# Kernel tuning notes

Hardware: AMD Instinct MI355X
Metric: run time of the kernel (lower is better)

The kernel has to match this reference:

```python
import jax, jax.numpy as jnp
import numpy as np

B, S, C = 8, 1024, 768
H = 12            # num_heads
HD = C // H       # head_dim = 64
QH = QW = 32      # input_size; QH*QW == S


def setup_inputs() -> dict:
    key = jax.random.key(0)
    ks = jax.random.split(key, 6)
    return {
        "x": jax.random.normal(ks[0], (B, S, C), dtype=jnp.float32),
        "w_qkv": jax.random.normal(ks[1], (3 * C, C), dtype=jnp.float32) * 0.02,
        "w_out": jax.random.normal(ks[2], (C, C), dtype=jnp.float32) * 0.02,
        "b_out": jax.random.normal(ks[3], (C,), dtype=jnp.float32) * 0.02,
        "rel_pos_h": jax.random.normal(ks[4], (2 * QH - 1, HD), dtype=jnp.float32) * 0.02,
        "rel_pos_w": jax.random.normal(ks[5], (2 * QW - 1, HD), dtype=jnp.float32) * 0.02,
    }


def reference(x, w_qkv, w_out, b_out, rel_pos_h, rel_pos_w):
    scale = HD ** -0.5
    # qkv projection (no bias), rearrange 'b s (qkv h d) -> qkv b h s d'
    qkv = (x @ w_qkv.T).reshape(B, S, 3, H, HD).transpose(2, 0, 3, 1, 4)
    q, k, v = qkv[0], qkv[1], qkv[2]            # each (B, H, S, HD)

    attn = jnp.einsum('bhxd,bhyd->bhxy', q, k) * scale  # (B, H, S, S)

    # decomposed relative position bias (q_size == k_size, no interpolation)
    idx = jnp.arange(QH)[:, None] - jnp.arange(QH)[None, :] + (QH - 1)
    Rh = rel_pos_h[idx]                          # (QH, QH, HD)
    Rw = rel_pos_w[idx]                          # (QW, QW, HD)
    rq = q.reshape(B * H, QH, QW, HD)
    rel_h = jnp.einsum('bhwc,hkc->bhwk', rq, Rh)  # (BH, QH, QW, QH)
    rel_w = jnp.einsum('bhwc,wkc->bhwk', rq, Rw)  # (BH, QH, QW, QW)
    attn = (attn.reshape(B * H, QH, QW, QH, QW)
            + rel_h[:, :, :, :, None]
            + rel_w[:, :, :, None, :]).reshape(B, H, S, S)

    attn = jax.nn.softmax(attn, axis=-1)
    out = jnp.einsum('bhxy,bhyd->bhxd', attn, v)  # (B, H, S, HD)
    out = out.transpose(0, 2, 1, 3).reshape(B, S, C)
    return out @ w_out.T + b_out
```

## Files before the change

### kernel.cpp

```cpp
#include <hip/hip_runtime.h>
#include <cstdint>
#include <math.h>


using u16 = unsigned short;
using bf16x8 = __attribute__((ext_vector_type(8))) short;
using f32x4  = __attribute__((ext_vector_type(4))) float;

#define LOG2E 1.44269504088896340736f

__device__ __forceinline__ float bf2f(u16 u) {
  union { uint32_t i; float f; } v; v.i = ((uint32_t)u) << 16; return v.f;
}
__device__ __forceinline__ u16 f2bf(float f) {
  union { float f; uint32_t i; } v; v.f = f;
  uint32_t r = v.i + 0x7FFFu + ((v.i >> 16) & 1u);
  return (u16)(r >> 16);
}
__device__ __forceinline__ uint32_t cvt2(float a, float b) {
#if __has_builtin(__builtin_amdgcn_cvt_pk_bf16_f32)
  return __builtin_bit_cast(uint32_t, __builtin_amdgcn_cvt_pk_bf16_f32(a, b));
#else
  return (uint32_t)f2bf(a) | ((uint32_t)f2bf(b) << 16);
#endif
}
__device__ __forceinline__ float fexp2(float x) {
#if __has_builtin(__builtin_amdgcn_exp2f)
  return __builtin_amdgcn_exp2f(x);
#else
  return exp2f(x);
#endif
}
__device__ __forceinline__ uint4 pack8(float4 a, float4 b) {
  uint4 r;
  r.x = cvt2(a.x, a.y); r.y = cvt2(a.z, a.w);
  r.z = cvt2(b.x, b.y); r.w = cvt2(b.z, b.w);
  return r;
}
union U4BF8 { uint4 u; bf16x8 v; };

__device__ __forceinline__ void load16_to_lds(const void* g, void* l) {
  auto gp = reinterpret_cast<const __attribute__((address_space(1))) uint32_t*>(
      reinterpret_cast<uintptr_t>(g));
  auto lp = reinterpret_cast<__attribute__((address_space(3))) uint32_t*>(
      reinterpret_cast<uintptr_t>(l));
  __builtin_amdgcn_global_load_lds(gp, lp, 16, 0, 0);
}

__global__ __launch_bounds__(256, 8)
void cvt_bf16(const float* __restrict__ s0, u16* __restrict__ d0, int n0,
              const float* __restrict__ s1, u16* __restrict__ d1, int n1,
              const float* __restrict__ s2, u16* __restrict__ d2)
{
  int i = (blockIdx.x*256 + threadIdx.x) * 8;
  const float* s; u16* d; int off;
  if (i < n0)            { s = s0; d = d0; off = i; }
  else if (i < n0 + n1)  { s = s1; d = d1; off = i - n0; }
  else                   { s = s2; d = d2; off = i - n0 - n1; }
  float4 a = *(const float4*)(s + off);
  float4 b = *(const float4*)(s + off + 4);
  *(uint4*)(d + off) = pack8(a, b);
}

__global__ __launch_bounds__(256, 4)
void qkv_gemm(const u16* __restrict__ xb, const u16* __restrict__ wqb,
              u16* __restrict__ Q, u16* __restrict__ K, u16* __restrict__ VT)
{
  __shared__ u16 sA[2][128*32];
  __shared__ u16 sB[2][128*32];
  const int tid  = threadIdx.x;
  const int lane = tid & 63, wid = tid >> 6;
  const int quad = lane >> 4, l16 = lane & 15;
  const int blk = blockIdx.x;
  const int tn = (blk >> 3) % 18;
  const int tm = (blk & 7) + (blk / 144) * 8;
  const int wm = wid & 1, wn = wid >> 1;

  const u16* gA[2]; const u16* gB[2];
  #pragma unroll
  for (int it = 0; it < 2; ++it) {
    int g = it*256 + tid;
    int row = g >> 2;
    int cg  = (g & 3) ^ ((row >> 1) & 3);
    gA[it] = xb  + (size_t)(tm*128 + row)*768 + cg*8;
    gB[it] = wqb + (size_t)(tn*128 + row)*768 + cg*8;
  }

  const f32x4 fz = {0.f, 0.f, 0.f, 0.f};
  f32x4 acc[4][4];
  #pragma unroll
  for (int i = 0; i < 4; ++i)
    #pragma unroll
    for (int j = 0; j < 4; ++j) acc[i][j] = fz;

  #pragma unroll
  for (int it = 0; it < 2; ++it) {
    load16_to_lds(gA[it], (char*)&sA[0][0] + (it*256 + tid)*16);
    load16_to_lds(gB[it], (char*)&sB[0][0] + (it*256 + tid)*16);
  }

  int cur = 0;
  for (int k = 0; k < 24; ++k) {
    if (k < 23) {
      const int k0 = (k + 1)*32;
      char* dA = (char*)&sA[cur ^ 1][0];
      char* dB = (char*)&sB[cur ^ 1][0];
      __builtin_amdgcn_sched_barrier(0);
      #pragma unroll
      for (int it = 0; it < 2; ++it) {
        load16_to_lds(gA[it] + k0, dA + (it*256 + tid)*16);
        load16_to_lds(gB[it] + k0, dB + (it*256 + tid)*16);
      }
      __builtin_amdgcn_sched_barrier(0);
      asm volatile("s_waitcnt vmcnt(4)" ::: "memory");
    } else {
      asm volatile("s_waitcnt vmcnt(0)" ::: "memory");
    }
    __builtin_amdgcn_s_barrier();
    __builtin_amdgcn_sched_barrier(0);

    const u16* sAc = &sA[cur][0];
    const u16* sBc = &sB[cur][0];
    bf16x8 af[4], bfv[4];
    #pragma unroll
    for (int mt = 0; mt < 4; ++mt) {
      int m = wm*64 + mt*16 + l16;
      af[mt] = *(const bf16x8*)&sAc[(m*4 + (quad ^ ((m >> 1) & 3)))*8];
    }
    #pragma unroll
    for (int nt = 0; nt < 4; ++nt) {
      int n = wn*64 + nt*16 + l16;
      bfv[nt] = *(const bf16x8*)&sBc[(n*4 + (quad ^ ((n >> 1) & 3)))*8];
    }
    __builtin_amdgcn_s_setprio(1);
    #pragma unroll
    for (int mt = 0; mt < 4; ++mt)
      #pragma unroll
      for (int nt = 0; nt < 4; ++nt)
        acc[mt][nt] = __builtin_amdgcn_mfma_f32_16x16x32_bf16(af[mt], bfv[nt], acc[mt][nt], 0, 0, 0);
    __builtin_amdgcn_s_setprio(0);
    __builtin_amdgcn_sched_barrier(0);
    __builtin_amdgcn_s_barrier();
    __builtin_amdgcn_sched_barrier(0);
    cur ^= 1;
  }

  const float KSCL = 0.125f * LOG2E;
  #pragma unroll
  for (int mt = 0; mt < 4; ++mt) {
    #pragma unroll
    for (int nt = 0; nt < 4; ++nt) {
      const int col = wn*64 + nt*16 + l16;
      const int n = tn*128 + col;
      #pragma unroll
      for (int r = 0; r < 4; ++r) {
        const int rowin = wm*64 + mt*16 + quad*4 + r;
        const int m = tm*128 + rowin;
        const int b = m >> 10, s = m & 1023;
        if (n < 768) {
          int h = n >> 6, d = n & 63;
          Q[(((size_t)b*12 + h)*1024 + s)*64 + d] = f2bf(acc[mt][nt][r]);
        } else if (n < 1536) {
          int nn = n - 768; int h = nn >> 6, d = nn & 63;
          int bh = b*12 + h;
          int kb = s >> 7, srel = s & 127;
          K[(size_t)bh*65536
            + (((kb*8 + (srel >> 4))*2 + (d >> 5))*4 + ((d >> 3) & 3))*128
            + (srel & 15)*8 + (d & 7)] = f2bf(acc[mt][nt][r] * KSCL);
        } else {
          int nn = n - 1536; int h = nn >> 6, d = nn & 63;
          int bh = b*12 + h;
          int kb = s >> 7, srel = s & 127;
          VT[(size_t)bh*65536
             + ((((kb*2 + (srel >> 6))*2 + ((srel >> 5) & 1))*4 + (d >> 4))*4 + ((srel >> 3) & 3))*128
             + (d & 15)*8 + (srel & 7)] = f2bf(acc[mt][nt][r]);
        }
      }
    }
  }
}

__global__ __launch_bounds__(256, 4)
void rel_bias(const u16* __restrict__ Q, const float* __restrict__ rph, const float* __restrict__ rpw,
              u16* __restrict__ RH, u16* __restrict__ RW)
{
  const int tid  = threadIdx.x;
  const int lane = tid & 63, wid = tid >> 6;
  const int quad = lane >> 4, l16 = lane & 15;
  const int blk = blockIdx.x;
  const int gx = (blk >> 3) & 7;
  const int bh = (blk & 7) + (blk >> 6) * 8;
  const bool isW = gx >= 4;
  const float* rp = isW ? rpw : rph;
  u16* RO = isW ? RW : RH;
  const int qb = (gx & 3)*8 + wid*2;
  const f32x4 fz = {0.f, 0.f, 0.f, 0.f};

  #pragma unroll
  for (int gi = 0; gi < 2; ++gi) {
    const int qv = qb + gi;
    f32x4 acc[2][2];
    #pragma unroll
    for (int i = 0; i < 2; ++i)
      #pragma unroll
      for (int j = 0; j < 2; ++j) acc[i][j] = fz;

    #pragma unroll
    for (int ks = 0; ks < 2; ++ks) {
      bf16x8 af[2], bfv[2];
      #pragma unroll
      for (int mt = 0; mt < 2; ++mt) {
        int m = mt*16 + l16;
        int xrow = isW ? (m*32 + qv) : (qv*32 + m);
        af[mt] = *(const bf16x8*)(Q + ((size_t)bh*1024 + xrow)*64 + ks*32 + quad*8);
      }
      #pragma unroll
      for (int nt = 0; nt < 2; ++nt) {
        int n = nt*16 + l16;
        const float* bp = rp + (size_t)(qv - n + 31)*64 + ks*32 + quad*8;
        U4BF8 c; c.u = pack8(*(const float4*)bp, *(const float4*)(bp + 4));
        bfv[nt] = c.v;
      }
      #pragma unroll
      for (int mt = 0; mt < 2; ++mt)
        #pragma unroll
        for (int nt = 0; nt < 2; ++nt)
          acc[mt][nt] = __builtin_amdgcn_mfma_f32_16x16x32_bf16(af[mt], bfv[nt], acc[mt][nt], 0, 0, 0);
    }
    #pragma unroll
    for (int mt = 0; mt < 2; ++mt)
      #pragma unroll
      for (int nt = 0; nt < 2; ++nt)
        #pragma unroll
        for (int r = 0; r < 4; ++r) {
          int j = mt*16 + quad*4 + r;
          int xrow = isW ? (j*32 + qv) : (qv*32 + j);
          int n = nt*16 + l16;
          RO[((size_t)bh*1024 + xrow)*32 + n] = f2bf(acc[mt][nt][r] * LOG2E);
        }
  }
}

__global__ __launch_bounds__(512, 4)
void attn_kernel(const u16* __restrict__ Q, const u16* __restrict__ KF, const u16* __restrict__ VF,
                 const u16* __restrict__ RH, const u16* __restrict__ RW, u16* __restrict__ AO)
{
  __shared__ u16 sK[2][8192];
  __shared__ u16 sV[2][8192];
  __shared__ u16 sP[128*64];
  const int tid  = threadIdx.x;
  const int lane = tid & 63, wid = tid >> 6;
  const int quad = lane >> 4, l16 = lane & 15;
  const int blk = blockIdx.x;
  const int qt = (blk >> 3) & 7;
  const int bh = (blk & 7) + (blk >> 6) * 8;
  const int q0 = qt * 128;
  const int ql = wid*16 + l16;

  bf16x8 qf[2];
  #pragma unroll
  for (int ks = 0; ks < 2; ++ks)
    qf[ks] = *(const bf16x8*)(Q + ((size_t)bh*1024 + q0 + ql)*64 + ks*32 + quad*8);

  const size_t ro = ((size_t)bh*1024 + q0 + ql)*32;
  float bwv[2][4];
  #pragma unroll
  for (int h2 = 0; h2 < 2; ++h2) {
    uint2 t = *(const uint2*)(RW + ro + h2*16 + quad*4);
    bwv[h2][0] = bf2f((u16)(t.x & 0xFFFF));
    bwv[h2][1] = bf2f((u16)(t.x >> 16));
    bwv[h2][2] = bf2f((u16)(t.y & 0xFFFF));
    bwv[h2][3] = bf2f((u16)(t.y >> 16));
  }

  const u16* KFs = KF + (size_t)bh*65536;
  const u16* VFs = VF + (size_t)bh*65536;

  load16_to_lds(KFs + tid*8,        (char*)&sK[0][0] + tid*16);
  load16_to_lds(KFs + 4096 + tid*8, (char*)&sK[0][0] + 8192 + tid*16);
  load16_to_lds(VFs + tid*8,        (char*)&sV[0][0] + tid*16);
  load16_to_lds(VFs + 4096 + tid*8, (char*)&sV[0][0] + 8192 + tid*16);

  const f32x4 fz = {0.f, 0.f, 0.f, 0.f};
  f32x4 lsv = fz;
  f32x4 accO[4];
  #pragma unroll
  for (int dt = 0; dt < 4; ++dt) accO[dt] = fz;

  int cur = 0;
  for (int kb = 0; kb < 8; ++kb) {
    uint2 bhl = *(const uint2*)(RH + ro + kb*4);

    if (kb < 7) {
      const u16* ks = KFs + (size_t)(kb + 1)*8192;
      const u16* vs = VFs + (size_t)(kb + 1)*8192;
      char* dk = (char*)&sK[cur ^ 1][0];
      char* dv = (char*)&sV[cur ^ 1][0];
      __builtin_amdgcn_sched_barrier(0);
      load16_to_lds(ks + tid*8,        dk + tid*16);
      load16_to_lds(ks + 4096 + tid*8, dk + 8192 + tid*16);
      load16_to_lds(vs + tid*8,        dv + tid*16);
      load16_to_lds(vs + 4096 + tid*8, dv + 8192 + tid*16);
      __builtin_amdgcn_sched_barrier(0);
      asm volatile("s_waitcnt vmcnt(4)" ::: "memory");
    } else {
      asm volatile("s_waitcnt vmcnt(0)" ::: "memory");
    }
    __builtin_amdgcn_s_barrier();
    __builtin_amdgcn_sched_barrier(0);

    const u16* sKc = &sK[cur][0];
    const u16* sVc = &sV[cur][0];

    #pragma unroll
    for (int h = 0; h < 2; ++h) {
      f32x4 sAcc[4];
      #pragma unroll
      for (int smt = 0; smt < 4; ++smt) {
        const int g = h*2 + (smt >> 1);
        const uint32_t gw = (g < 2) ? bhl.x : bhl.y;
        const float bhf = bf2f((u16)(gw >> ((g & 1)*16)));
        #pragma unroll
        for (int r = 0; r < 4; ++r) sAcc[smt][r] = bhf + bwv[smt & 1][r];
      }
      __builtin_amdgcn_s_setprio(1);
      #pragma unroll
      for (int ks = 0; ks < 2; ++ks) {
        #pragma unroll
        for (int smt = 0; smt < 4; ++smt) {
          bf16x8 af = *(const bf16x8*)&sKc[(size_t)(((h*4 + smt)*2 + ks))*512 + lane*8];
          sAcc[smt] = __builtin_amdgcn_mfma_f32_16x16x32_bf16(af, qf[ks], sAcc[smt], 0, 0, 0);
        }
      }
      __builtin_amdgcn_s_setprio(0);

      #pragma unroll
      for (int smt = 0; smt < 4; ++smt) {
        #pragma unroll
        for (int r = 0; r < 4; ++r) {
          float p = fexp2(sAcc[smt][r]);
          sAcc[smt][r] = p;
          lsv[r] += p;
        }
      }

      #pragma unroll
      for (int smt = 0; smt < 4; ++smt) {
        uint2 w;
        w.x = cvt2(sAcc[smt][0], sAcc[smt][1]);
        w.y = cvt2(sAcc[smt][2], sAcc[smt][3]);
        const int sg = smt*2 + (quad >> 1);
        *(uint2*)&sP[ql*64 + ((sg ^ (ql & 7))*8) + (quad & 1)*4] = w;
      }

      #pragma unroll
      for (int ka = 0; ka < 2; ++ka) {
        bf16x8 pf = *(const bf16x8*)&sP[ql*64 + (((ka*4 + quad) ^ (ql & 7))*8)];
        __builtin_amdgcn_s_setprio(1);
        #pragma unroll
        for (int dt = 0; dt < 4; ++dt) {
          bf16x8 vf = *(const bf16x8*)&sVc[(size_t)(((h*2 + ka)*4 + dt))*512 + lane*8];
          accO[dt] = __builtin_amdgcn_mfma_f32_16x16x32_bf16(vf, pf, accO[dt], 0, 0, 0);
        }
        __builtin_amdgcn_s_setprio(0);
      }
    }

    __builtin_amdgcn_sched_barrier(0);
    __builtin_amdgcn_s_barrier();
    __builtin_amdgcn_sched_barrier(0);
    cur ^= 1;
  }

  const int b = bh / 12, head = bh % 12;
  float s = lsv[0] + lsv[1] + lsv[2] + lsv[3];
  s += __shfl_xor(s, 16);
  s += __shfl_xor(s, 32);
  const float inv = 1.f / s;
  const size_t base = ((size_t)(b*1024 + q0 + ql))*768 + head*64;
  #pragma unroll
  for (int dt = 0; dt < 4; ++dt) {
    uint2 o;
    o.x = cvt2(accO[dt][0]*inv, accO[dt][1]*inv);
    o.y = cvt2(accO[dt][2]*inv, accO[dt][3]*inv);
    *(uint2*)&AO[base + dt*16 + quad*4] = o;
  }
}

__global__ __launch_bounds__(256, 4)
void out_gemm(const u16* __restrict__ A, const u16* __restrict__ wob, const float* __restrict__ bout,
              float* __restrict__ out)
{
  __shared__ u16 sA[2][128*32];
  __shared__ u16 sB[2][128*32];
  const int tid  = threadIdx.x;
  const int lane = tid & 63, wid = tid >> 6;
  const int quad = lane >> 4, l16 = lane & 15;
  const int blk = blockIdx.x;
  const int tn = (blk >> 3) % 6;
  const int tm = (blk & 7) + (blk / 48) * 8;
  const int wm = wid & 1, wn = wid >> 1;

  const u16* gA[2]; const u16* gB[2];
  #pragma unroll
  for (int it = 0; it < 2; ++it) {
    int g = it*256 + tid;
    int row = g >> 2;
    int cg  = (g & 3) ^ ((row >> 1) & 3);
    gA[it] = A   + (size_t)(tm*128 + row)*768 + cg*8;
    gB[it] = wob + (size_t)(tn*128 + row)*768 + cg*8;
  }

  const f32x4 fz = {0.f, 0.f, 0.f, 0.f};
  f32x4 acc[4][4];
  #pragma unroll
  for (int i = 0; i < 4; ++i)
    #pragma unroll
    for (int j = 0; j < 4; ++j) acc[i][j] = fz;

  #pragma unroll
  for (int it = 0; it < 2; ++it) {
    load16_to_lds(gA[it], (char*)&sA[0][0] + (it*256 + tid)*16);
    load16_to_lds(gB[it], (char*)&sB[0][0] + (it*256 + tid)*16);
  }

  int cur = 0;
  for (int k = 0; k < 24; ++k) {
    if (k < 23) {
      const int k0 = (k + 1)*32;
      char* dA = (char*)&sA[cur ^ 1][0];
      char* dB = (char*)&sB[cur ^ 1][0];
      __builtin_amdgcn_sched_barrier(0);
      #pragma unroll
      for (int it = 0; it < 2; ++it) {
        load16_to_lds(gA[it] + k0, dA + (it*256 + tid)*16);
        load16_to_lds(gB[it] + k0, dB + (it*256 + tid)*16);
      }
      __builtin_amdgcn_sched_barrier(0);
      asm volatile("s_waitcnt vmcnt(4)" ::: "memory");
    } else {
      asm volatile("s_waitcnt vmcnt(0)" ::: "memory");
    }
    __builtin_amdgcn_s_barrier();
    __builtin_amdgcn_sched_barrier(0);

    const u16* sAc = &sA[cur][0];
    const u16* sBc = &sB[cur][0];
    bf16x8 af[4], bfv[4];
    #pragma unroll
    for (int mt = 0; mt < 4; ++mt) {
      int m = wm*64 + mt*16 + l16;
      af[mt] = *(const bf16x8*)&sAc[(m*4 + (quad ^ ((m >> 1) & 3)))*8];
    }
    #pragma unroll
    for (int nt = 0; nt < 4; ++nt) {
      int n = wn*64 + nt*16 + l16;
      bfv[nt] = *(const bf16x8*)&sBc[(n*4 + (quad ^ ((n >> 1) & 3)))*8];
    }
    __builtin_amdgcn_s_setprio(1);
    #pragma unroll
    for (int mt = 0; mt < 4; ++mt)
      #pragma unroll
      for (int nt = 0; nt < 4; ++nt)
        acc[mt][nt] = __builtin_amdgcn_mfma_f32_16x16x32_bf16(af[mt], bfv[nt], acc[mt][nt], 0, 0, 0);
    __builtin_amdgcn_s_setprio(0);
    __builtin_amdgcn_sched_barrier(0);
    __builtin_amdgcn_s_barrier();
    __builtin_amdgcn_sched_barrier(0);
    cur ^= 1;
  }

  #pragma unroll
  for (int mt = 0; mt < 4; ++mt) {
    #pragma unroll
    for (int nt = 0; nt < 4; ++nt) {
      const int n = tn*128 + wn*64 + nt*16 + l16;
      const float bv = bout[n];
      #pragma unroll
      for (int r = 0; r < 4; ++r) {
        const int rowin = wm*64 + mt*16 + quad*4 + r;
        out[(size_t)(tm*128 + rowin)*768 + n] = acc[mt][nt][r] + bv;
      }
    }
  }
}

extern "C" void kernel_launch(void* const* d_in, const int* in_sizes, int n_in,
                              void* d_out, int out_size, void* d_ws, size_t ws_size,
                              hipStream_t stream)
{
  const float* x    = (const float*)d_in[0];
  const float* wqkv = (const float*)d_in[1];
  const float* wout = (const float*)d_in[2];
  const float* bout = (const float*)d_in[3];
  const float* rph  = (const float*)d_in[4];
  const float* rpw  = (const float*)d_in[5];
  float* out = (float*)d_out;

  char* ws = (char*)d_ws;
  const size_t SZ = (size_t)96*1024*64;
  u16* Q   = (u16*)ws;
  u16* K   = Q  + SZ;
  u16* VT  = K  + SZ;
  u16* RH  = VT + SZ;
  u16* RW  = RH + (size_t)96*1024*32;
  u16* AO  = RW + (size_t)96*1024*32;
  u16* xb  = AO + SZ;
  u16* wqb = xb + SZ;
  u16* wob = wqb + (size_t)2304*768;

  const int n0 = 8192*768, n1 = 2304*768;
  cvt_bf16   <<<dim3(4224), dim3(256), 0, stream>>>(x, xb, n0, wqkv, wqb, n1, wout, wob);
  qkv_gemm   <<<dim3(1152), dim3(256), 0, stream>>>(xb, wqb, Q, K, VT);
  rel_bias   <<<dim3(768),  dim3(256), 0, stream>>>(Q, rph, rpw, RH, RW);
  attn_kernel<<<dim3(768),  dim3(512), 0, stream>>>(Q, K, VT, RH, RW, AO);
  out_gemm   <<<dim3(384),  dim3(256), 0, stream>>>(AO, wob, bout, out);
}
```

Before: 206.1 us.

## Pre-pack weights into MFMA fragment layout and load B operands directly to registers

Adds a conversion kernel that writes both weight matrices in per-lane MFMA fragment order, so the QKV and output GEMMs can read the B operand straight from global memory into registers, prefetched one k-step ahead. This removes the B shared-memory staging and its LDS reads. The A operand moves to a triple-buffered LDS ring, which lets the trailing per-iteration barrier go. The cost is more vector-memory traffic per wave (each wave fetches its own B fragments), more registers, an extra kernel launch, and reliance on the triple buffer for safety without the second barrier.

```diff
diff --git a/kernel.cpp b/kernel.cpp
--- a/kernel.cpp
+++ b/kernel.cpp
@@ -48,26 +48,42 @@
 }
 
 __global__ __launch_bounds__(256, 8)
-void cvt_bf16(const float* __restrict__ s0, u16* __restrict__ d0, int n0,
-              const float* __restrict__ s1, u16* __restrict__ d1, int n1,
-              const float* __restrict__ s2, u16* __restrict__ d2)
+void cvt_bf16(const float* __restrict__ s0, u16* __restrict__ d0)
 {
   int i = (blockIdx.x*256 + threadIdx.x) * 8;
-  const float* s; u16* d; int off;
-  if (i < n0)            { s = s0; d = d0; off = i; }
-  else if (i < n0 + n1)  { s = s1; d = d1; off = i - n0; }
-  else                   { s = s2; d = d2; off = i - n0 - n1; }
-  float4 a = *(const float4*)(s + off);
-  float4 b = *(const float4*)(s + off + 4);
-  *(uint4*)(d + off) = pack8(a, b);
+  float4 a = *(const float4*)(s0 + i);
+  float4 b = *(const float4*)(s0 + i + 4);
+  *(uint4*)(d0 + i) = pack8(a, b);
+}
+
+__global__ __launch_bounds__(256, 8)
+void cvt_wfrag(const float* __restrict__ wqkv, const float* __restrict__ wout,
+               u16* __restrict__ WQF, u16* __restrict__ WOF)
+{
+  int t = blockIdx.x*256 + threadIdx.x;
+  int lane = t & 63;
+  int f = t >> 6;
+  int nf = f & 7;
+  int kstep = (f >> 3) % 24;
+  int panel = f / 192;
+  int l16 = lane & 15, quad = lane >> 4;
+  int k = kstep*32 + quad*8;
+  const float* src; u16* dst; int pl, n;
+  if (panel < 18) { src = wqkv; dst = WQF; pl = panel; }
+  else            { src = wout; dst = WOF; pl = panel - 18; }
+  n = pl*128 + nf*16 + l16;
+  const float* p = src + (size_t)n*768 + k;
+  float4 a = *(const float4*)p;
+  float4 b = *(const float4*)(p + 4);
+  size_t off = ((size_t)pl*192 + kstep*8 + nf)*512 + (size_t)lane*8;
+  *(uint4*)(dst + off) = pack8(a, b);
 }
 
 __global__ __launch_bounds__(256, 4)
-void qkv_gemm(const u16* __restrict__ xb, const u16* __restrict__ wqb,
+void qkv_gemm(const u16* __restrict__ xb, const u16* __restrict__ wqf,
               u16* __restrict__ Q, u16* __restrict__ K, u16* __restrict__ VT)
 {
-  __shared__ u16 sA[2][128*32];
-  __shared__ u16 sB[2][128*32];
+  __shared__ u16 sA[3][128*32];
   const int tid  = threadIdx.x;
   const int lane = tid & 63, wid = tid >> 6;
   const int quad = lane >> 4, l16 = lane & 15;
@@ -76,15 +92,15 @@
   const int tm = (blk & 7) + (blk / 144) * 8;
   const int wm = wid & 1, wn = wid >> 1;
 
-  const u16* gA[2]; const u16* gB[2];
+  const u16* gA[2];
   #pragma unroll
   for (int it = 0; it < 2; ++it) {
     int g = it*256 + tid;
     int row = g >> 2;
     int cg  = (g & 3) ^ ((row >> 1) & 3);
-    gA[it] = xb  + (size_t)(tm*128 + row)*768 + cg*8;
-    gB[it] = wqb + (size_t)(tn*128 + row)*768 + cg*8;
-  }
+    gA[it] = xb + (size_t)(tm*128 + row)*768 + cg*8;
+  }
+  const u16* gB = wqf + ((size_t)tn*192 + wn*4)*512 + (size_t)lane*8;
 
   const f32x4 fz = {0.f, 0.f, 0.f, 0.f};
   f32x4 acc[4][4];
@@ -94,25 +110,28 @@
     for (int j = 0; j < 4; ++j) acc[i][j] = fz;
 
   #pragma unroll
-  for (int it = 0; it < 2; ++it) {
+  for (int it = 0; it < 2; ++it)
     load16_to_lds(gA[it], (char*)&sA[0][0] + (it*256 + tid)*16);
-    load16_to_lds(gB[it], (char*)&sB[0][0] + (it*256 + tid)*16);
-  }
+  bf16x8 bc[4], bn[4];
+  #pragma unroll
+  for (int nt = 0; nt < 4; ++nt)
+    bc[nt] = *(const bf16x8*)(gB + (size_t)nt*512);
 
   int cur = 0;
   for (int k = 0; k < 24; ++k) {
     if (k < 23) {
       const int k0 = (k + 1)*32;
-      char* dA = (char*)&sA[cur ^ 1][0];
-      char* dB = (char*)&sB[cur ^ 1][0];
+      int nb = cur + 1; if (nb >= 3) nb -= 3;
+      char* dA = (char*)&sA[nb][0];
       __builtin_amdgcn_sched_barrier(0);
       #pragma unroll
-      for (int it = 0; it < 2; ++it) {
+      for (int it = 0; it < 2; ++it)
         load16_to_lds(gA[it] + k0, dA + (it*256 + tid)*16);
-        load16_to_lds(gB[it] + k0, dB + (it*256 + tid)*16);
-      }
+      #pragma unroll
+      for (int nt = 0; nt < 4; ++nt)
+        bn[nt] = *(const bf16x8*)(gB + ((size_t)(k + 1)*8 + nt)*512);
       __builtin_amdgcn_sched_barrier(0);
-      asm volatile("s_waitcnt vmcnt(4)" ::: "memory");
+      asm volatile("s_waitcnt vmcnt(6)" ::: "memory");
     } else {
       asm volatile("s_waitcnt vmcnt(0)" ::: "memory");
     }
@@ -120,29 +139,25 @@
     __builtin_amdgcn_sched_barrier(0);
 
     const u16* sAc = &sA[cur][0];
-    const u16* sBc = &sB[cur][0];
-    bf16x8 af[4], bfv[4];
+    bf16x8 af[4];
     #pragma unroll
     for (int mt = 0; mt < 4; ++mt) {
       int m = wm*64 + mt*16 + l16;
       af[mt] = *(const bf16x8*)&sAc[(m*4 + (quad ^ ((m >> 1) & 3)))*8];
     }
-    #pragma unroll
-    for (int nt = 0; nt < 4; ++nt) {
-      int n = wn*64 + nt*16 + l16;
-      bfv[nt] = *(const bf16x8*)&sBc[(n*4 + (quad ^ ((n >> 1) & 3)))*8];
-    }
     __builtin_amdgcn_s_setprio(1);
     #pragma unroll
     for (int mt = 0; mt < 4; ++mt)
       #pragma unroll
       for (int nt = 0; nt < 4; ++nt)
-        acc[mt][nt] = __builtin_amdgcn_mfma_f32_16x16x32_bf16(af[mt], bfv[nt], acc[mt][nt], 0, 0, 0);
+        acc[mt][nt] = __builtin_amdgcn_mfma_f32_16x16x32_bf16(af[mt], bc[nt], acc[mt][nt], 0, 0, 0);
     __builtin_amdgcn_s_setprio(0);
-    __builtin_amdgcn_sched_barrier(0);
-    __builtin_amdgcn_s_barrier();
-    __builtin_amdgcn_sched_barrier(0);
-    cur ^= 1;
+    if (k < 23) {
+      #pragma unroll
+      for (int nt = 0; nt < 4; ++nt) bc[nt] = bn[nt];
+    }
+    __builtin_amdgcn_sched_barrier(0);
+    cur += 1; if (cur >= 3) cur = 0;
   }
 
   const float KSCL = 0.125f * LOG2E;
@@ -388,11 +403,10 @@
 }
 
 __global__ __launch_bounds__(256, 4)
-void out_gemm(const u16* __restrict__ A, const u16* __restrict__ wob, const float* __restrict__ bout,
+void out_gemm(const u16* __restrict__ A, const u16* __restrict__ wof, const float* __restrict__ bout,
               float* __restrict__ out)
 {
-  __shared__ u16 sA[2][128*32];
-  __shared__ u16 sB[2][128*32];
+  __shared__ u16 sA[3][128*32];
   const int tid  = threadIdx.x;
   const int lane = tid & 63, wid = tid >> 6;
   const int quad = lane >> 4, l16 = lane & 15;
@@ -401,15 +415,15 @@
   const int tm = (blk & 7) + (blk / 48) * 8;
   const int wm = wid & 1, wn = wid >> 1;
 
-  const u16* gA[2]; const u16* gB[2];
+  const u16* gA[2];
   #pragma unroll
   for (int it = 0; it < 2; ++it) {
     int g = it*256 + tid;
     int row = g >> 2;
     int cg  = (g & 3) ^ ((row >> 1) & 3);
-    gA[it] = A   + (size_t)(tm*128 + row)*768 + cg*8;
-    gB[it] = wob + (size_t)(tn*128 + row)*768 + cg*8;
-  }
+    gA[it] = A + (size_t)(tm*128 + row)*768 + cg*8;
+  }
+  const u16* gB = wof + ((size_t)tn*192 + wn*4)*512 + (size_t)lane*8;
 
   const f32x4 fz = {0.f, 0.f, 0.f, 0.f};
   f32x4 acc[4][4];
@@ -419,25 +433,28 @@
     for (int j = 0; j < 4; ++j) acc[i][j] = fz;
 
   #pragma unroll
-  for (int it = 0; it < 2; ++it) {
+  for (int it = 0; it < 2; ++it)
     load16_to_lds(gA[it], (char*)&sA[0][0] + (it*256 + tid)*16);
-    load16_to_lds(gB[it], (char*)&sB[0][0] + (it*256 + tid)*16);
-  }
+  bf16x8 bc[4], bn[4];
+  #pragma unroll
+  for (int nt = 0; nt < 4; ++nt)
+    bc[nt] = *(const bf16x8*)(gB + (size_t)nt*512);
 
   int cur = 0;
   for (int k = 0; k < 24; ++k) {
     if (k < 23) {
       const int k0 = (k + 1)*32;
-      char* dA = (char*)&sA[cur ^ 1][0];
-      char* dB = (char*)&sB[cur ^ 1][0];
+      int nb = cur + 1; if (nb >= 3) nb -= 3;
+      char* dA = (char*)&sA[nb][0];
       __builtin_amdgcn_sched_barrier(0);
       #pragma unroll
-      for (int it = 0; it < 2; ++it) {
+      for (int it = 0; it < 2; ++it)
         load16_to_lds(gA[it] + k0, dA + (it*256 + tid)*16);
-        load16_to_lds(gB[it] + k0, dB + (it*256 + tid)*16);
-      }
+      #pragma unroll
+      for (int nt = 0; nt < 4; ++nt)
+        bn[nt] = *(const bf16x8*)(gB + ((size_t)(k + 1)*8 + nt)*512);
       __builtin_amdgcn_sched_barrier(0);
-      asm volatile("s_waitcnt vmcnt(4)" ::: "memory");
+      asm volatile("s_waitcnt vmcnt(6)" ::: "memory");
     } else {
       asm volatile("s_waitcnt vmcnt(0)" ::: "memory");
     }
@@ -445,29 +462,25 @@
     __builtin_amdgcn_sched_barrier(0);
 
     const u16* sAc = &sA[cur][0];
-    const u16* sBc = &sB[cur][0];
-    bf16x8 af[4], bfv[4];
+    bf16x8 af[4];
     #pragma unroll
     for (int mt = 0; mt < 4; ++mt) {
       int m = wm*64 + mt*16 + l16;
       af[mt] = *(const bf16x8*)&sAc[(m*4 + (quad ^ ((m >> 1) & 3)))*8];
     }
-    #pragma unroll
-    for (int nt = 0; nt < 4; ++nt) {
-      int n = wn*64 + nt*16 + l16;
-      bfv[nt] = *(const bf16x8*)&sBc[(n*4 + (quad ^ ((n >> 1) & 3)))*8];
-    }
     __builtin_amdgcn_s_setprio(1);
     #pragma unroll
     for (int mt = 0; mt < 4; ++mt)
       #pragma unroll
       for (int nt = 0; nt < 4; ++nt)
-        acc[mt][nt] = __builtin_amdgcn_mfma_f32_16x16x32_bf16(af[mt], bfv[nt], acc[mt][nt], 0, 0, 0);
+        acc[mt][nt] = __builtin_amdgcn_mfma_f32_16x16x32_bf16(af[mt], bc[nt], acc[mt][nt], 0, 0, 0);
     __builtin_amdgcn_s_setprio(0);
-    __builtin_amdgcn_sched_barrier(0);
-    __builtin_amdgcn_s_barrier();
-    __builtin_amdgcn_sched_barrier(0);
-    cur ^= 1;
+    if (k < 23) {
+      #pragma unroll
+      for (int nt = 0; nt < 4; ++nt) bc[nt] = bn[nt];
+    }
+    __builtin_amdgcn_sched_barrier(0);
+    cur += 1; if (cur >= 3) cur = 0;
   }
 
   #pragma unroll
@@ -506,13 +519,13 @@
   u16* RW  = RH + (size_t)96*1024*32;
   u16* AO  = RW + (size_t)96*1024*32;
   u16* xb  = AO + SZ;
-  u16* wqb = xb + SZ;
-  u16* wob = wqb + (size_t)2304*768;
-
-  const int n0 = 8192*768, n1 = 2304*768;
-  cvt_bf16   <<<dim3(4224), dim3(256), 0, stream>>>(x, xb, n0, wqkv, wqb, n1, wout, wob);
-  qkv_gemm   <<<dim3(1152), dim3(256), 0, stream>>>(xb, wqb, Q, K, VT);
+  u16* wqf = xb + SZ;
+  u16* wof = wqf + (size_t)2304*768;
+
+  cvt_bf16   <<<dim3(3072), dim3(256), 0, stream>>>(x, xb);
+  cvt_wfrag  <<<dim3(1152), dim3(256), 0, stream>>>(wqkv, wout, wqf, wof);
+  qkv_gemm   <<<dim3(1152), dim3(256), 0, stream>>>(xb, wqf, Q, K, VT);
   rel_bias   <<<dim3(768),  dim3(256), 0, stream>>>(Q, rph, rpw, RH, RW);
   attn_kernel<<<dim3(768),  dim3(512), 0, stream>>>(Q, K, VT, RH, RW, AO);
-  out_gemm   <<<dim3(384),  dim3(256), 0, stream>>>(AO, wob, bout, out);
-}
+  out_gemm   <<<dim3(384),  dim3(256), 0, stream>>>(AO, wof, bout, out);
+}
```

After: 208.7 us. No clear change (+1.3%).
